# Performance work log

Measured on AMD Instinct MI355X. Metric: run time of the kernel, lower is better.

Reference implementation:

```python
import jax, jax.numpy as jnp
import numpy as np

B, S, D_IN, H, D_OUT = 2048, 256, 3, 128, 6
DT = 0.1


def setup_inputs() -> dict:
    key = jax.random.key(0)
    ks = jax.random.split(key, 7)
    sx = 1.0 / np.sqrt(D_IN)
    sh = 1.0 / np.sqrt(H)
    return {
        "x": jax.random.normal(ks[0], (B, S, D_IN), dtype=jnp.float32),
        "W_xh": jax.random.uniform(ks[1], (H, D_IN), jnp.float32, -sx, sx),
        "W_hh": jax.random.uniform(ks[2], (H, H), jnp.float32, -sh, sh),
        "b_hh": jax.random.uniform(ks[3], (H,), jnp.float32, -sh, sh),
        "log_tau": jnp.zeros((H,), jnp.float32),
        "fc_W": jax.random.uniform(ks[4], (D_OUT, H), jnp.float32, -sh, sh),
        "fc_b": jax.random.uniform(ks[5], (D_OUT,), jnp.float32, -sh, sh),
    }


def reference(x, W_xh, W_hh, b_hh, log_tau, fc_W, fc_b):
    # tau is time-invariant: compute once outside the scan
    tau = jax.nn.softplus(log_tau) + 0.001  # [H]
    # precompute input projections for all timesteps (one big GEMM)
    xp = jnp.einsum("bsd,hd->sbh", x, W_xh)  # [S, B, H]

    def step(h, xt_proj):
        f = jnp.tanh(xt_proj + h @ W_hh.T + b_hh)  # [B, H]
        h = h + (-h + f) / tau * DT
        return h, None

    h0 = jnp.zeros((x.shape[0], W_hh.shape[0]), dtype=x.dtype)
    hT, _ = jax.lax.scan(step, h0, xp)
    params = jax.nn.softplus(hT @ fc_W.T + fc_b)  # [B, 6]
    return params
```

## Files before the change

### kernel.cpp

```cpp
#include <hip/hip_runtime.h>
#include <math.h>

#define B_TOT 2048
#define S_LEN 256
#define DIN   3
#define H     128
#define DOUT  6
#define DT_C  0.1f

#define NROWS 8
#define HPAD  136
#define PPAD  132

#define PRESCALE 2.8853900817779268f

typedef __attribute__((ext_vector_type(8))) short short8;
typedef __attribute__((ext_vector_type(4))) float f32x4;

__device__ __forceinline__ unsigned short f2bf(float f) {
  unsigned int u = __float_as_uint(f);
  u += 0x7FFFu + ((u >> 16) & 1u);
  return (unsigned short)(u >> 16);
}
__device__ __forceinline__ unsigned int pack2_bf16(float a, float b) {
  unsigned int ua = __float_as_uint(a), ub = __float_as_uint(b);
  ua = ua + 0x7FFFu + ((ua >> 16) & 1u);
  ub = ub + 0x7FFFu + ((ub >> 16) & 1u);
  return (ua >> 16) | (ub & 0xFFFF0000u);
}
__device__ __forceinline__ float dpp_xor8(float v) {
  int i = __float_as_int(v);
  int r = __builtin_amdgcn_update_dpp(i, i, 0x128 , 0xF, 0xF, false);
  return __int_as_float(r);
}

__launch_bounds__(512, 2)
__global__ void ltc_kernel(const float* __restrict__ x,
                           const float* __restrict__ W_xh,
                           const float* __restrict__ W_hh,
                           const float* __restrict__ b_hh,
                           const float* __restrict__ log_tau,
                           const float* __restrict__ fc_W,
                           const float* __restrict__ fc_b,
                           float* __restrict__ out) {
  __shared__ alignas(16) unsigned short sh_h[2][NROWS][HPAD];
  __shared__ alignas(16) float sh_p[NROWS][PPAD];

  const int tid  = threadIdx.x;
  const int w    = tid >> 6;
  const int lane = tid & 63;
  const int quad = lane >> 4;
  const int l16  = lane & 15;
  const int rb0  = blockIdx.x * NROWS;

  {
    uint4* p = (uint4*)&sh_h[0][0][0];
    const int n16 = (2 * NROWS * HPAD) / 8;
    for (int i = tid; i < n16; i += 512) p[i] = make_uint4(0, 0, 0, 0);
  }

  short8 wa[4];
  {
    const int j = w * 16 + l16;
#pragma unroll
    for (int kc = 0; kc < 4; ++kc) {
      const float* src = W_hh + j * H + kc * 32 + quad * 8;
#pragma unroll
      for (int i = 0; i < 8; ++i)
        wa[kc][i] = (short)f2bf(src[i] * PRESCALE);
    }
  }

  const int brow = l16 & 7;
  const int rbse = (l16 >> 3) * 2;
  float ewx[2][3], ebh[2], ecc[2], ea[2], encc2[2];
#pragma unroll
  for (int r = 0; r < 2; ++r) {
    const int j = w * 16 + quad * 4 + rbse + r;
    ewx[r][0] = W_xh[j * 3 + 0] * PRESCALE;
    ewx[r][1] = W_xh[j * 3 + 1] * PRESCALE;
    ewx[r][2] = W_xh[j * 3 + 2] * PRESCALE;
    ebh[r]    = b_hh[j] * PRESCALE;
    float lt  = log_tau[j];
    float tau = logf(1.f + expf(lt)) + 0.001f;
    float cc  = DT_C / tau;
    ecc[r]    = cc;
    ea[r]     = 1.f - cc;
    encc2[r]  = -2.f * cc;
  }
  const bool lowhalf = (l16 < 8);
  const float* xp = x + (size_t)(rb0 + brow) * (S_LEN * DIN);

  float hreg[2] = {0.f, 0.f};

  const int rd_off = l16 * HPAD + quad * 8;
  const int wr_off = brow * HPAD + w * 16 + quad * 4 + rbse;
  const unsigned short* __restrict__ buf0 = &sh_h[0][0][0];
  unsigned short* __restrict__ buf1 = &sh_h[1][0][0];

  short8 bf[4];
#pragma unroll
  for (int kc = 0; kc < 4; ++kc) bf[kc] = short8{0, 0, 0, 0, 0, 0, 0, 0};

  float2 pfa = *(const float2*)(xp);
  float2 pfb = *(const float2*)(xp + 2);
  float2 pfc = *(const float2*)(xp + 4);

  __syncthreads();

  auto do_step = [&](const unsigned short* __restrict__ cur,
                     unsigned short* __restrict__ nxt,
                     float xc0, float xc1, float xc2) {
    if (l16 < NROWS) {
#pragma unroll
      for (int kc = 0; kc < 4; ++kc)
        bf[kc] = *(const short8*)(cur + rd_off + kc * 32);
    }

    float t0 = __builtin_fmaf(xc2, ewx[0][2], ebh[0]);
    t0 = __builtin_fmaf(xc1, ewx[0][1], t0);
    t0 = __builtin_fmaf(xc0, ewx[0][0], t0);
    float t1 = __builtin_fmaf(xc2, ewx[1][2], ebh[1]);
    t1 = __builtin_fmaf(xc1, ewx[1][1], t1);
    t1 = __builtin_fmaf(xc0, ewx[1][0], t1);

    f32x4 ah = {0.f, 0.f, 0.f, 0.f};
#pragma unroll
    for (int kc = 0; kc < 4; ++kc)
      ah = __builtin_amdgcn_mfma_f32_16x16x32_bf16(wa[kc], bf[kc], ah, 0, 0, 0);

    float d2 = dpp_xor8(ah[2]);
    float d3 = dpp_xor8(ah[3]);
    float pre0 = lowhalf ? ah[0] : d2;
    float pre1 = lowhalf ? ah[1] : d3;

    {
      float e  = __builtin_amdgcn_exp2f(pre0 + t0);
      float rc = __builtin_amdgcn_rcpf(e + 1.f);
      hreg[0] = __builtin_fmaf(encc2[0], rc, __builtin_fmaf(hreg[0], ea[0], ecc[0]));
    }
    {
      float e  = __builtin_amdgcn_exp2f(pre1 + t1);
      float rc = __builtin_amdgcn_rcpf(e + 1.f);
      hreg[1] = __builtin_fmaf(encc2[1], rc, __builtin_fmaf(hreg[1], ea[1], ecc[1]));
    }

    *(unsigned int*)(nxt + wr_off) = pack2_bf16(hreg[0], hreg[1]);
    __syncthreads();
  };

  for (int s = 0; s < S_LEN; s += 2) {
    float2 xa = pfa, xb = pfb, xc = pfc;
    if (s + 2 < S_LEN) {
      xp += 6;
      pfa = *(const float2*)(xp);
      pfb = *(const float2*)(xp + 2);
      pfc = *(const float2*)(xp + 4);
    }
    do_step(buf0, buf1, xa.x, xa.y, xb.x);
    do_step(buf1, (unsigned short*)buf0, xb.y, xc.x, xc.y);
  }

  {
    float2 v = make_float2(hreg[0], hreg[1]);
    *(float2*)&sh_p[brow][w * 16 + quad * 4 + rbse] = v;
  }
  __syncthreads();

  if (tid < NROWS * DOUT) {
    const int b = tid / DOUT;
    const int o = tid - b * DOUT;
    const float* fw = fc_W + o * H;
    float acc = fc_b[o];
#pragma unroll 4
    for (int k = 0; k < H; ++k) acc += sh_p[b][k] * fw[k];
    float sp = (acc > 15.f) ? acc : logf(1.f + expf(acc));
    out[(rb0 + b) * DOUT + o] = sp;
  }
}

extern "C" void kernel_launch(void* const* d_in, const int* in_sizes, int n_in,
                              void* d_out, int out_size, void* d_ws, size_t ws_size,
                              hipStream_t stream) {
  const float* x       = (const float*)d_in[0];
  const float* W_xh    = (const float*)d_in[1];
  const float* W_hh    = (const float*)d_in[2];
  const float* b_hh    = (const float*)d_in[3];
  const float* log_tau = (const float*)d_in[4];
  const float* fc_W    = (const float*)d_in[5];
  const float* fc_b    = (const float*)d_in[6];
  float* out           = (float*)d_out;

  ltc_kernel<<<dim3(B_TOT / NROWS), dim3(512), 0, stream>>>(
      x, W_xh, W_hh, b_hh, log_tau, fc_W, fc_b, out);
}
```

Before: 144.8 us.

## Halve rows per block, split MFMA chain, one hidden unit per lane

Reduces batch rows per workgroup from 8 to 4, doubling the grid to 512 blocks and raising launch bounds to 4 blocks per CU. Each lane now owns a single hidden unit, extracted from the MFMA accumulators with three DPP rotations and selects. The four dependent MFMAs are split into two independent accumulator chains to shorten latency. Other changes: hardware bf16 conversion, a deeper two-step prefetch of x, and a lighter barrier. It trades more blocks and padding for lower per-step serial latency, and pays with extra DPP/select work and unused MFMA columns.

```diff
diff --git a/kernel.cpp b/kernel.cpp
--- a/kernel.cpp
+++ b/kernel.cpp
@@ -8,8 +8,8 @@
 #define DOUT  6
 #define DT_C  0.1f
 
-#define NROWS 8
-#define HPAD  136
+#define NROWS 4
+#define HPAD  144
 #define PPAD  132
 
 #define PRESCALE 2.8853900817779268f
@@ -17,24 +17,24 @@
 typedef __attribute__((ext_vector_type(8))) short short8;
 typedef __attribute__((ext_vector_type(4))) float f32x4;
 
-__device__ __forceinline__ unsigned short f2bf(float f) {
-  unsigned int u = __float_as_uint(f);
-  u += 0x7FFFu + ((u >> 16) & 1u);
-  return (unsigned short)(u >> 16);
-}
-__device__ __forceinline__ unsigned int pack2_bf16(float a, float b) {
-  unsigned int ua = __float_as_uint(a), ub = __float_as_uint(b);
-  ua = ua + 0x7FFFu + ((ua >> 16) & 1u);
-  ub = ub + 0x7FFFu + ((ub >> 16) & 1u);
-  return (ua >> 16) | (ub & 0xFFFF0000u);
-}
-__device__ __forceinline__ float dpp_xor8(float v) {
+template<int CTRL>
+__device__ __forceinline__ float dpp_rot(float v) {
   int i = __float_as_int(v);
-  int r = __builtin_amdgcn_update_dpp(i, i, 0x128 , 0xF, 0xF, false);
+  int r = __builtin_amdgcn_update_dpp(i, i, CTRL, 0xF, 0xF, false);
   return __int_as_float(r);
 }
 
-__launch_bounds__(512, 2)
+__device__ __forceinline__ unsigned short cvt_bf16(float a) {
+  unsigned int r;
+  asm("v_cvt_pk_bf16_f32 %0, %1, %2" : "=v"(r) : "v"(a), "v"(a));
+  return (unsigned short)r;
+}
+
+__device__ __forceinline__ void lds_barrier() {
+  asm volatile("s_waitcnt lgkmcnt(0)\n\ts_barrier" ::: "memory");
+}
+
+__launch_bounds__(512, 4)
 __global__ void ltc_kernel(const float* __restrict__ x,
                            const float* __restrict__ W_xh,
                            const float* __restrict__ W_hh,
@@ -51,6 +51,8 @@
   const int lane = tid & 63;
   const int quad = lane >> 4;
   const int l16  = lane & 15;
+  const int brow = l16 & 3;
+  const int sel  = l16 >> 2;
   const int rb0  = blockIdx.x * NROWS;
 
   {
@@ -61,110 +63,102 @@
 
   short8 wa[4];
   {
-    const int j = w * 16 + l16;
+    const int jj = w * 16 + l16;
 #pragma unroll
     for (int kc = 0; kc < 4; ++kc) {
-      const float* src = W_hh + j * H + kc * 32 + quad * 8;
+      const float* src = W_hh + jj * H + kc * 32 + quad * 8;
 #pragma unroll
       for (int i = 0; i < 8; ++i)
-        wa[kc][i] = (short)f2bf(src[i] * PRESCALE);
+        wa[kc][i] = (short)cvt_bf16(src[i] * PRESCALE);
     }
   }
 
-  const int brow = l16 & 7;
-  const int rbse = (l16 >> 3) * 2;
-  float ewx[2][3], ebh[2], ecc[2], ea[2], encc2[2];
-#pragma unroll
-  for (int r = 0; r < 2; ++r) {
-    const int j = w * 16 + quad * 4 + rbse + r;
-    ewx[r][0] = W_xh[j * 3 + 0] * PRESCALE;
-    ewx[r][1] = W_xh[j * 3 + 1] * PRESCALE;
-    ewx[r][2] = W_xh[j * 3 + 2] * PRESCALE;
-    ebh[r]    = b_hh[j] * PRESCALE;
-    float lt  = log_tau[j];
-    float tau = logf(1.f + expf(lt)) + 0.001f;
-    float cc  = DT_C / tau;
-    ecc[r]    = cc;
-    ea[r]     = 1.f - cc;
-    encc2[r]  = -2.f * cc;
+  const int j = w * 16 + quad * 4 + sel;
+  const float ewx0 = W_xh[j * 3 + 0] * PRESCALE;
+  const float ewx1 = W_xh[j * 3 + 1] * PRESCALE;
+  const float ewx2 = W_xh[j * 3 + 2] * PRESCALE;
+  const float ebh  = b_hh[j] * PRESCALE;
+  float tau, ecc, ea, encc2;
+  {
+    float lt = log_tau[j];
+    tau   = logf(1.f + expf(lt)) + 0.001f;
+    ecc   = DT_C / tau;
+    ea    = 1.f - ecc;
+    encc2 = -2.f * ecc;
   }
-  const bool lowhalf = (l16 < 8);
-  const float* xp = x + (size_t)(rb0 + brow) * (S_LEN * DIN);
 
-  float hreg[2] = {0.f, 0.f};
+  float hreg = 0.f;
 
-  const int rd_off = l16 * HPAD + quad * 8;
-  const int wr_off = brow * HPAD + w * 16 + quad * 4 + rbse;
-  const unsigned short* __restrict__ buf0 = &sh_h[0][0][0];
+  const int rd_off = brow * HPAD + quad * 8;
+  const int wr_off = brow * HPAD + j;
+  unsigned short* __restrict__ buf0 = &sh_h[0][0][0];
   unsigned short* __restrict__ buf1 = &sh_h[1][0][0];
 
-  short8 bf[4];
-#pragma unroll
-  for (int kc = 0; kc < 4; ++kc) bf[kc] = short8{0, 0, 0, 0, 0, 0, 0, 0};
-
-  float2 pfa = *(const float2*)(xp);
-  float2 pfb = *(const float2*)(xp + 2);
-  float2 pfc = *(const float2*)(xp + 4);
+  const float* xq = x + (size_t)(rb0 + brow) * (S_LEN * DIN);
+  float2 pa0 = *(const float2*)(xq);
+  float2 pb0 = *(const float2*)(xq + 2);
+  float2 pc0 = *(const float2*)(xq + 4);
+  float2 pa1 = *(const float2*)(xq + 6);
+  float2 pb1 = *(const float2*)(xq + 8);
+  float2 pc1 = *(const float2*)(xq + 10);
+  xq += 12;
 
   __syncthreads();
 
-  auto do_step = [&](const unsigned short* __restrict__ cur,
+  auto do_step = [&](unsigned short* __restrict__ cur,
                      unsigned short* __restrict__ nxt,
                      float xc0, float xc1, float xc2) {
-    if (l16 < NROWS) {
-#pragma unroll
-      for (int kc = 0; kc < 4; ++kc)
-        bf[kc] = *(const short8*)(cur + rd_off + kc * 32);
-    }
+    short8 b0 = *(const short8*)(cur + rd_off);
+    short8 b1 = *(const short8*)(cur + rd_off + 32);
+    short8 b2 = *(const short8*)(cur + rd_off + 64);
+    short8 b3 = *(const short8*)(cur + rd_off + 96);
 
-    float t0 = __builtin_fmaf(xc2, ewx[0][2], ebh[0]);
-    t0 = __builtin_fmaf(xc1, ewx[0][1], t0);
-    t0 = __builtin_fmaf(xc0, ewx[0][0], t0);
-    float t1 = __builtin_fmaf(xc2, ewx[1][2], ebh[1]);
-    t1 = __builtin_fmaf(xc1, ewx[1][1], t1);
-    t1 = __builtin_fmaf(xc0, ewx[1][0], t1);
+    float t = __builtin_fmaf(xc2, ewx2, ebh);
+    t = __builtin_fmaf(xc1, ewx1, t);
+    t = __builtin_fmaf(xc0, ewx0, t);
 
-    f32x4 ah = {0.f, 0.f, 0.f, 0.f};
-#pragma unroll
-    for (int kc = 0; kc < 4; ++kc)
-      ah = __builtin_amdgcn_mfma_f32_16x16x32_bf16(wa[kc], bf[kc], ah, 0, 0, 0);
+    f32x4 a0 = {0.f, 0.f, 0.f, 0.f};
+    f32x4 a1 = {0.f, 0.f, 0.f, 0.f};
+    a0 = __builtin_amdgcn_mfma_f32_16x16x32_bf16(wa[0], b0, a0, 0, 0, 0);
+    a1 = __builtin_amdgcn_mfma_f32_16x16x32_bf16(wa[2], b2, a1, 0, 0, 0);
+    a0 = __builtin_amdgcn_mfma_f32_16x16x32_bf16(wa[1], b1, a0, 0, 0, 0);
+    a1 = __builtin_amdgcn_mfma_f32_16x16x32_bf16(wa[3], b3, a1, 0, 0, 0);
 
-    float d2 = dpp_xor8(ah[2]);
-    float d3 = dpp_xor8(ah[3]);
-    float pre0 = lowhalf ? ah[0] : d2;
-    float pre1 = lowhalf ? ah[1] : d3;
+    const float d0 = a0[0] + a1[0];
+    const float d1 = a0[1] + a1[1];
+    const float d2 = a0[2] + a1[2];
+    const float d3 = a0[3] + a1[3];
 
-    {
-      float e  = __builtin_amdgcn_exp2f(pre0 + t0);
-      float rc = __builtin_amdgcn_rcpf(e + 1.f);
-      hreg[0] = __builtin_fmaf(encc2[0], rc, __builtin_fmaf(hreg[0], ea[0], ecc[0]));
-    }
-    {
-      float e  = __builtin_amdgcn_exp2f(pre1 + t1);
-      float rc = __builtin_amdgcn_rcpf(e + 1.f);
-      hreg[1] = __builtin_fmaf(encc2[1], rc, __builtin_fmaf(hreg[1], ea[1], ecc[1]));
-    }
+    float r1 = dpp_rot<0x12C>(d1);
+    float r2 = dpp_rot<0x128>(d2);
+    float r3 = dpp_rot<0x124>(d3);
+    float pre = d0;
+    pre = (sel == 1) ? r1 : pre;
+    pre = (sel == 2) ? r2 : pre;
+    pre = (sel == 3) ? r3 : pre;
 
-    *(unsigned int*)(nxt + wr_off) = pack2_bf16(hreg[0], hreg[1]);
-    __syncthreads();
+    float e  = __builtin_amdgcn_exp2f(pre + t);
+    float rc = __builtin_amdgcn_rcpf(e + 1.f);
+    hreg = __builtin_fmaf(encc2, rc, __builtin_fmaf(hreg, ea, ecc));
+
+    *(unsigned short*)(nxt + wr_off) = cvt_bf16(hreg);
+    lds_barrier();
   };
 
   for (int s = 0; s < S_LEN; s += 2) {
-    float2 xa = pfa, xb = pfb, xc = pfc;
-    if (s + 2 < S_LEN) {
-      xp += 6;
-      pfa = *(const float2*)(xp);
-      pfb = *(const float2*)(xp + 2);
-      pfc = *(const float2*)(xp + 4);
+    float2 xa = pa0, xb = pb0, xc = pc0;
+    pa0 = pa1; pb0 = pb1; pc0 = pc1;
+    if (s + 4 < S_LEN) {
+      pa1 = *(const float2*)(xq);
+      pb1 = *(const float2*)(xq + 2);
+      pc1 = *(const float2*)(xq + 4);
+      xq += 6;
     }
     do_step(buf0, buf1, xa.x, xa.y, xb.x);
-    do_step(buf1, (unsigned short*)buf0, xb.y, xc.x, xc.y);
+    do_step(buf1, buf0, xb.y, xc.x, xc.y);
   }
 
-  {
-    float2 v = make_float2(hreg[0], hreg[1]);
-    *(float2*)&sh_p[brow][w * 16 + quad * 4 + rbse] = v;
-  }
+  sh_p[brow][j] = hreg;
   __syncthreads();
 
   if (tid < NROWS * DOUT) {
```

Measured after the change: 196.4 us. 1.36x slower.

## Swizzle hidden-state LDS layout, split MFMA chains, use hardware bf16 pack and lighter barrier

Applied to the files above, without the earlier changes.

Changes the shared-memory layout of the bf16 hidden state so each MFMA B-operand read is contiguous per quad/lane, removing the padded row layout. Splits the four dependent MFMAs into two independent accumulator chains summed at the end, shortening the per-step dependency latency. Replaces software bf16 rounding with the v_cvt_pk_bf16_f32 instruction and the full __syncthreads with an inline waitcnt+s_barrier. Deepens x prefetch by one more step pair. The inline-asm barrier relies on correct lgkmcnt semantics, and the split adds a few VALU adds per step.

```diff
diff --git a/kernel.cpp b/kernel.cpp
--- a/kernel.cpp
+++ b/kernel.cpp
@@ -9,7 +9,6 @@
 #define DT_C  0.1f
 
 #define NROWS 8
-#define HPAD  136
 #define PPAD  132
 
 #define PRESCALE 2.8853900817779268f
@@ -17,21 +16,20 @@
 typedef __attribute__((ext_vector_type(8))) short short8;
 typedef __attribute__((ext_vector_type(4))) float f32x4;
 
-__device__ __forceinline__ unsigned short f2bf(float f) {
-  unsigned int u = __float_as_uint(f);
-  u += 0x7FFFu + ((u >> 16) & 1u);
-  return (unsigned short)(u >> 16);
-}
-__device__ __forceinline__ unsigned int pack2_bf16(float a, float b) {
-  unsigned int ua = __float_as_uint(a), ub = __float_as_uint(b);
-  ua = ua + 0x7FFFu + ((ua >> 16) & 1u);
-  ub = ub + 0x7FFFu + ((ub >> 16) & 1u);
-  return (ua >> 16) | (ub & 0xFFFF0000u);
-}
 __device__ __forceinline__ float dpp_xor8(float v) {
   int i = __float_as_int(v);
   int r = __builtin_amdgcn_update_dpp(i, i, 0x128 , 0xF, 0xF, false);
   return __int_as_float(r);
+}
+
+__device__ __forceinline__ unsigned int cvt_pk_bf16(float a, float b) {
+  unsigned int r;
+  asm("v_cvt_pk_bf16_f32 %0, %1, %2" : "=v"(r) : "v"(a), "v"(b));
+  return r;
+}
+
+__device__ __forceinline__ void lds_barrier() {
+  asm volatile("s_waitcnt lgkmcnt(0)\n\ts_barrier" ::: "memory");
 }
 
 __launch_bounds__(512, 2)
@@ -43,7 +41,7 @@
                            const float* __restrict__ fc_W,
                            const float* __restrict__ fc_b,
                            float* __restrict__ out) {
-  __shared__ alignas(16) unsigned short sh_h[2][NROWS][HPAD];
+  __shared__ alignas(16) unsigned short sh_h[2][1024];
   __shared__ alignas(16) float sh_p[NROWS][PPAD];
 
   const int tid  = threadIdx.x;
@@ -54,29 +52,32 @@
   const int rb0  = blockIdx.x * NROWS;
 
   {
-    uint4* p = (uint4*)&sh_h[0][0][0];
-    const int n16 = (2 * NROWS * HPAD) / 8;
+    uint4* p = (uint4*)&sh_h[0][0];
+    const int n16 = (2 * 1024) / 8;
     for (int i = tid; i < n16; i += 512) p[i] = make_uint4(0, 0, 0, 0);
   }
 
   short8 wa[4];
   {
-    const int j = w * 16 + l16;
+    const int jj = w * 16 + l16;
 #pragma unroll
     for (int kc = 0; kc < 4; ++kc) {
-      const float* src = W_hh + j * H + kc * 32 + quad * 8;
-#pragma unroll
-      for (int i = 0; i < 8; ++i)
-        wa[kc][i] = (short)f2bf(src[i] * PRESCALE);
+      const float* src = W_hh + jj * H + kc * 32 + quad * 8;
+#pragma unroll
+      for (int i = 0; i < 8; ++i) {
+        unsigned int pk = cvt_pk_bf16(src[i] * PRESCALE, 0.f);
+        wa[kc][i] = (short)(pk & 0xFFFFu);
+      }
     }
   }
 
   const int brow = l16 & 7;
   const int rbse = (l16 >> 3) * 2;
+  const int j0   = w * 16 + quad * 4 + rbse;
   float ewx[2][3], ebh[2], ecc[2], ea[2], encc2[2];
 #pragma unroll
   for (int r = 0; r < 2; ++r) {
-    const int j = w * 16 + quad * 4 + rbse + r;
+    const int j = j0 + r;
     ewx[r][0] = W_xh[j * 3 + 0] * PRESCALE;
     ewx[r][1] = W_xh[j * 3 + 1] * PRESCALE;
     ewx[r][2] = W_xh[j * 3 + 2] * PRESCALE;
@@ -93,18 +94,23 @@
 
   float hreg[2] = {0.f, 0.f};
 
-  const int rd_off = l16 * HPAD + quad * 8;
-  const int wr_off = brow * HPAD + w * 16 + quad * 4 + rbse;
-  const unsigned short* __restrict__ buf0 = &sh_h[0][0][0];
-  unsigned short* __restrict__ buf1 = &sh_h[1][0][0];
+  const int rd_off = quad * 64 + l16 * 8;
+  const int wr_off = (j0 >> 5) * 256 + ((j0 >> 3) & 3) * 64 + brow * 8 + (j0 & 7);
+  unsigned short* __restrict__ buf0 = &sh_h[0][0];
+  unsigned short* __restrict__ buf1 = &sh_h[1][0];
 
   short8 bf[4];
 #pragma unroll
   for (int kc = 0; kc < 4; ++kc) bf[kc] = short8{0, 0, 0, 0, 0, 0, 0, 0};
 
-  float2 pfa = *(const float2*)(xp);
-  float2 pfb = *(const float2*)(xp + 2);
-  float2 pfc = *(const float2*)(xp + 4);
+  const float* xq = xp;
+  float2 pa0 = *(const float2*)(xq);
+  float2 pb0 = *(const float2*)(xq + 2);
+  float2 pc0 = *(const float2*)(xq + 4);
+  float2 pa1 = *(const float2*)(xq + 6);
+  float2 pb1 = *(const float2*)(xq + 8);
+  float2 pc1 = *(const float2*)(xq + 10);
+  xq += 12;
 
   __syncthreads();
 
@@ -114,7 +120,7 @@
     if (l16 < NROWS) {
 #pragma unroll
       for (int kc = 0; kc < 4; ++kc)
-        bf[kc] = *(const short8*)(cur + rd_off + kc * 32);
+        bf[kc] = *(const short8*)(cur + rd_off + kc * 256);
     }
 
     float t0 = __builtin_fmaf(xc2, ewx[0][2], ebh[0]);
@@ -124,15 +130,22 @@
     t1 = __builtin_fmaf(xc1, ewx[1][1], t1);
     t1 = __builtin_fmaf(xc0, ewx[1][0], t1);
 
-    f32x4 ah = {0.f, 0.f, 0.f, 0.f};
-#pragma unroll
-    for (int kc = 0; kc < 4; ++kc)
-      ah = __builtin_amdgcn_mfma_f32_16x16x32_bf16(wa[kc], bf[kc], ah, 0, 0, 0);
-
-    float d2 = dpp_xor8(ah[2]);
-    float d3 = dpp_xor8(ah[3]);
-    float pre0 = lowhalf ? ah[0] : d2;
-    float pre1 = lowhalf ? ah[1] : d3;
+    f32x4 a0 = {0.f, 0.f, 0.f, 0.f};
+    f32x4 a1 = {0.f, 0.f, 0.f, 0.f};
+    a0 = __builtin_amdgcn_mfma_f32_16x16x32_bf16(wa[0], bf[0], a0, 0, 0, 0);
+    a1 = __builtin_amdgcn_mfma_f32_16x16x32_bf16(wa[2], bf[2], a1, 0, 0, 0);
+    a0 = __builtin_amdgcn_mfma_f32_16x16x32_bf16(wa[1], bf[1], a0, 0, 0, 0);
+    a1 = __builtin_amdgcn_mfma_f32_16x16x32_bf16(wa[3], bf[3], a1, 0, 0, 0);
+
+    const float d0 = a0[0] + a1[0];
+    const float d1 = a0[1] + a1[1];
+    const float d2 = a0[2] + a1[2];
+    const float d3 = a0[3] + a1[3];
+
+    float e2 = dpp_xor8(d2);
+    float e3 = dpp_xor8(d3);
+    float pre0 = lowhalf ? d0 : e2;
+    float pre1 = lowhalf ? d1 : e3;
 
     {
       float e  = __builtin_amdgcn_exp2f(pre0 + t0);
@@ -145,25 +158,26 @@
       hreg[1] = __builtin_fmaf(encc2[1], rc, __builtin_fmaf(hreg[1], ea[1], ecc[1]));
     }
 
-    *(unsigned int*)(nxt + wr_off) = pack2_bf16(hreg[0], hreg[1]);
-    __syncthreads();
+    *(unsigned int*)(nxt + wr_off) = cvt_pk_bf16(hreg[0], hreg[1]);
+    lds_barrier();
   };
 
   for (int s = 0; s < S_LEN; s += 2) {
-    float2 xa = pfa, xb = pfb, xc = pfc;
-    if (s + 2 < S_LEN) {
-      xp += 6;
-      pfa = *(const float2*)(xp);
-      pfb = *(const float2*)(xp + 2);
-      pfc = *(const float2*)(xp + 4);
+    float2 xa = pa0, xb = pb0, xc = pc0;
+    pa0 = pa1; pb0 = pb1; pc0 = pc1;
+    if (s + 4 < S_LEN) {
+      pa1 = *(const float2*)(xq);
+      pb1 = *(const float2*)(xq + 2);
+      pc1 = *(const float2*)(xq + 4);
+      xq += 6;
     }
     do_step(buf0, buf1, xa.x, xa.y, xb.x);
-    do_step(buf1, (unsigned short*)buf0, xb.y, xc.x, xc.y);
+    do_step(buf1, buf0, xb.y, xc.x, xc.y);
   }
 
   {
     float2 v = make_float2(hreg[0], hreg[1]);
-    *(float2*)&sh_p[brow][w * 16 + quad * 4 + rbse] = v;
+    *(float2*)&sh_p[brow][j0] = v;
   }
   __syncthreads();
 
```

Result: slower. 186.2 us (+28.6%).

## Process 16 batch rows per block with 4 waves each owning 32 hidden units

Applied to the files above, without the earlier changes.

Each block now handles 16 sequence rows instead of 8 and uses 4 waves instead of 8. Each wave computes two 16-row M-tiles, so the MFMA N dimension is fully used rather than half-padded. The hidden state moves to an unpadded swizzled LDS layout that matches the MFMA B-operand, and the manual bf16 rounding is replaced with the hardware v_cvt_pk_bf16_f32 instruction. The block count halves to 128, so fewer workgroups are spread over the CUs. In exchange there is more per-wave work, with two independent accumulator chains, and fewer barriers per row processed.

```diff
diff --git a/kernel.cpp b/kernel.cpp
--- a/kernel.cpp
+++ b/kernel.cpp
@@ -8,8 +8,7 @@
 #define DOUT  6
 #define DT_C  0.1f
 
-#define NROWS 8
-#define HPAD  136
+#define NROWS 16
 #define PPAD  132
 
 #define PRESCALE 2.8853900817779268f
@@ -17,24 +16,13 @@
 typedef __attribute__((ext_vector_type(8))) short short8;
 typedef __attribute__((ext_vector_type(4))) float f32x4;
 
-__device__ __forceinline__ unsigned short f2bf(float f) {
-  unsigned int u = __float_as_uint(f);
-  u += 0x7FFFu + ((u >> 16) & 1u);
-  return (unsigned short)(u >> 16);
+__device__ __forceinline__ unsigned int cvt_pk_bf16(float a, float b) {
+  unsigned int r;
+  asm("v_cvt_pk_bf16_f32 %0, %1, %2" : "=v"(r) : "v"(a), "v"(b));
+  return r;
 }
-__device__ __forceinline__ unsigned int pack2_bf16(float a, float b) {
-  unsigned int ua = __float_as_uint(a), ub = __float_as_uint(b);
-  ua = ua + 0x7FFFu + ((ua >> 16) & 1u);
-  ub = ub + 0x7FFFu + ((ub >> 16) & 1u);
-  return (ua >> 16) | (ub & 0xFFFF0000u);
-}
-__device__ __forceinline__ float dpp_xor8(float v) {
-  int i = __float_as_int(v);
-  int r = __builtin_amdgcn_update_dpp(i, i, 0x128 , 0xF, 0xF, false);
-  return __int_as_float(r);
-}
-
-__launch_bounds__(512, 2)
+
+__launch_bounds__(256, 1)
 __global__ void ltc_kernel(const float* __restrict__ x,
                            const float* __restrict__ W_xh,
                            const float* __restrict__ W_hh,
@@ -43,7 +31,7 @@
                            const float* __restrict__ fc_W,
                            const float* __restrict__ fc_b,
                            float* __restrict__ out) {
-  __shared__ alignas(16) unsigned short sh_h[2][NROWS][HPAD];
+  __shared__ alignas(16) unsigned short sh_h[2][2048];
   __shared__ alignas(16) float sh_p[NROWS][PPAD];
 
   const int tid  = threadIdx.x;
@@ -54,54 +42,54 @@
   const int rb0  = blockIdx.x * NROWS;
 
   {
-    uint4* p = (uint4*)&sh_h[0][0][0];
-    const int n16 = (2 * NROWS * HPAD) / 8;
-    for (int i = tid; i < n16; i += 512) p[i] = make_uint4(0, 0, 0, 0);
-  }
-
-  short8 wa[4];
-  {
-    const int j = w * 16 + l16;
+    uint4* p = (uint4*)&sh_h[0][0];
+    for (int i = tid; i < 512; i += 256) p[i] = make_uint4(0, 0, 0, 0);
+  }
+
+  short8 wa[2][4];
+#pragma unroll
+  for (int mt = 0; mt < 2; ++mt) {
 #pragma unroll
     for (int kc = 0; kc < 4; ++kc) {
-      const float* src = W_hh + j * H + kc * 32 + quad * 8;
+      const float* src = W_hh + (w * 32 + mt * 16 + l16) * H + kc * 32 + quad * 8;
 #pragma unroll
       for (int i = 0; i < 8; ++i)
-        wa[kc][i] = (short)f2bf(src[i] * PRESCALE);
-    }
-  }
-
-  const int brow = l16 & 7;
-  const int rbse = (l16 >> 3) * 2;
-  float ewx[2][3], ebh[2], ecc[2], ea[2], encc2[2];
-#pragma unroll
-  for (int r = 0; r < 2; ++r) {
-    const int j = w * 16 + quad * 4 + rbse + r;
-    ewx[r][0] = W_xh[j * 3 + 0] * PRESCALE;
-    ewx[r][1] = W_xh[j * 3 + 1] * PRESCALE;
-    ewx[r][2] = W_xh[j * 3 + 2] * PRESCALE;
-    ebh[r]    = b_hh[j] * PRESCALE;
-    float lt  = log_tau[j];
-    float tau = logf(1.f + expf(lt)) + 0.001f;
-    float cc  = DT_C / tau;
-    ecc[r]    = cc;
-    ea[r]     = 1.f - cc;
-    encc2[r]  = -2.f * cc;
-  }
-  const bool lowhalf = (l16 < 8);
-  const float* xp = x + (size_t)(rb0 + brow) * (S_LEN * DIN);
-
-  float hreg[2] = {0.f, 0.f};
-
-  const int rd_off = l16 * HPAD + quad * 8;
-  const int wr_off = brow * HPAD + w * 16 + quad * 4 + rbse;
-  const unsigned short* __restrict__ buf0 = &sh_h[0][0][0];
-  unsigned short* __restrict__ buf1 = &sh_h[1][0][0];
-
-  short8 bf[4];
-#pragma unroll
-  for (int kc = 0; kc < 4; ++kc) bf[kc] = short8{0, 0, 0, 0, 0, 0, 0, 0};
-
+        wa[mt][kc][i] = (short)(cvt_pk_bf16(src[i] * PRESCALE, 0.f) & 0xFFFFu);
+    }
+  }
+
+  float ewx[2][4][3], ebh[2][4], ecc[2][4], ea[2][4], encc2[2][4];
+#pragma unroll
+  for (int mt = 0; mt < 2; ++mt) {
+#pragma unroll
+    for (int r = 0; r < 4; ++r) {
+      const int j = w * 32 + mt * 16 + quad * 4 + r;
+      ewx[mt][r][0] = W_xh[j * 3 + 0] * PRESCALE;
+      ewx[mt][r][1] = W_xh[j * 3 + 1] * PRESCALE;
+      ewx[mt][r][2] = W_xh[j * 3 + 2] * PRESCALE;
+      ebh[mt][r]    = b_hh[j] * PRESCALE;
+      float lt  = log_tau[j];
+      float tau = logf(1.f + expf(lt)) + 0.001f;
+      float cc  = DT_C / tau;
+      ecc[mt][r]   = cc;
+      ea[mt][r]    = 1.f - cc;
+      encc2[mt][r] = -2.f * cc;
+    }
+  }
+
+  float hreg[2][4];
+#pragma unroll
+  for (int mt = 0; mt < 2; ++mt)
+#pragma unroll
+    for (int r = 0; r < 4; ++r) hreg[mt][r] = 0.f;
+
+  const int rd_off  = quad * 128 + l16 * 8;
+  const int wr_off0 = (w * 64 + (0 * 2 + (quad >> 1)) * 16 + l16) * 8 + (quad & 1) * 4;
+  const int wr_off1 = (w * 64 + (1 * 2 + (quad >> 1)) * 16 + l16) * 8 + (quad & 1) * 4;
+  unsigned short* __restrict__ buf0 = &sh_h[0][0];
+  unsigned short* __restrict__ buf1 = &sh_h[1][0];
+
+  const float* xp = x + (size_t)(rb0 + l16) * (S_LEN * DIN);
   float2 pfa = *(const float2*)(xp);
   float2 pfb = *(const float2*)(xp + 2);
   float2 pfc = *(const float2*)(xp + 4);
@@ -111,41 +99,59 @@
   auto do_step = [&](const unsigned short* __restrict__ cur,
                      unsigned short* __restrict__ nxt,
                      float xc0, float xc1, float xc2) {
-    if (l16 < NROWS) {
-#pragma unroll
-      for (int kc = 0; kc < 4; ++kc)
-        bf[kc] = *(const short8*)(cur + rd_off + kc * 32);
-    }
-
-    float t0 = __builtin_fmaf(xc2, ewx[0][2], ebh[0]);
-    t0 = __builtin_fmaf(xc1, ewx[0][1], t0);
-    t0 = __builtin_fmaf(xc0, ewx[0][0], t0);
-    float t1 = __builtin_fmaf(xc2, ewx[1][2], ebh[1]);
-    t1 = __builtin_fmaf(xc1, ewx[1][1], t1);
-    t1 = __builtin_fmaf(xc0, ewx[1][0], t1);
-
-    f32x4 ah = {0.f, 0.f, 0.f, 0.f};
-#pragma unroll
-    for (int kc = 0; kc < 4; ++kc)
-      ah = __builtin_amdgcn_mfma_f32_16x16x32_bf16(wa[kc], bf[kc], ah, 0, 0, 0);
-
-    float d2 = dpp_xor8(ah[2]);
-    float d3 = dpp_xor8(ah[3]);
-    float pre0 = lowhalf ? ah[0] : d2;
-    float pre1 = lowhalf ? ah[1] : d3;
+    short8 b0 = *(const short8*)(cur + rd_off);
+    short8 b1 = *(const short8*)(cur + rd_off + 512);
+    short8 b2 = *(const short8*)(cur + rd_off + 1024);
+    short8 b3 = *(const short8*)(cur + rd_off + 1536);
+
+    float t[2][4];
+#pragma unroll
+    for (int mt = 0; mt < 2; ++mt)
+#pragma unroll
+      for (int r = 0; r < 4; ++r) {
+        float v = __builtin_fmaf(xc2, ewx[mt][r][2], ebh[mt][r]);
+        v = __builtin_fmaf(xc1, ewx[mt][r][1], v);
+        t[mt][r] = __builtin_fmaf(xc0, ewx[mt][r][0], v);
+      }
+
+    f32x4 aA0 = {0.f, 0.f, 0.f, 0.f}, aB0 = {0.f, 0.f, 0.f, 0.f};
+    f32x4 aA1 = {0.f, 0.f, 0.f, 0.f}, aB1 = {0.f, 0.f, 0.f, 0.f};
+    aA0 = __builtin_amdgcn_mfma_f32_16x16x32_bf16(wa[0][0], b0, aA0, 0, 0, 0);
+    aA1 = __builtin_amdgcn_mfma_f32_16x16x32_bf16(wa[1][0], b0, aA1, 0, 0, 0);
+    aB0 = __builtin_amdgcn_mfma_f32_16x16x32_bf16(wa[0][2], b2, aB0, 0, 0, 0);
+    aB1 = __builtin_amdgcn_mfma_f32_16x16x32_bf16(wa[1][2], b2, aB1, 0, 0, 0);
+    aA0 = __builtin_amdgcn_mfma_f32_16x16x32_bf16(wa[0][1], b1, aA0, 0, 0, 0);
+    aA1 = __builtin_amdgcn_mfma_f32_16x16x32_bf16(wa[1][1], b1, aA1, 0, 0, 0);
+    aB0 = __builtin_amdgcn_mfma_f32_16x16x32_bf16(wa[0][3], b3, aB0, 0, 0, 0);
+    aB1 = __builtin_amdgcn_mfma_f32_16x16x32_bf16(wa[1][3], b3, aB1, 0, 0, 0);
+
+#pragma unroll
+    for (int r = 0; r < 4; ++r) {
+      {
+        float pre = aA0[r] + aB0[r];
+        float e   = __builtin_amdgcn_exp2f(pre + t[0][r]);
+        float rc  = __builtin_amdgcn_rcpf(e + 1.f);
+        hreg[0][r] = __builtin_fmaf(encc2[0][r], rc,
+                     __builtin_fmaf(hreg[0][r], ea[0][r], ecc[0][r]));
+      }
+      {
+        float pre = aA1[r] + aB1[r];
+        float e   = __builtin_amdgcn_exp2f(pre + t[1][r]);
+        float rc  = __builtin_amdgcn_rcpf(e + 1.f);
+        hreg[1][r] = __builtin_fmaf(encc2[1][r], rc,
+                     __builtin_fmaf(hreg[1][r], ea[1][r], ecc[1][r]));
+      }
+    }
 
     {
-      float e  = __builtin_amdgcn_exp2f(pre0 + t0);
-      float rc = __builtin_amdgcn_rcpf(e + 1.f);
-      hreg[0] = __builtin_fmaf(encc2[0], rc, __builtin_fmaf(hreg[0], ea[0], ecc[0]));
-    }
-    {
-      float e  = __builtin_amdgcn_exp2f(pre1 + t1);
-      float rc = __builtin_amdgcn_rcpf(e + 1.f);
-      hreg[1] = __builtin_fmaf(encc2[1], rc, __builtin_fmaf(hreg[1], ea[1], ecc[1]));
-    }
-
-    *(unsigned int*)(nxt + wr_off) = pack2_bf16(hreg[0], hreg[1]);
+      uint2 v0, v1;
+      v0.x = cvt_pk_bf16(hreg[0][0], hreg[0][1]);
+      v0.y = cvt_pk_bf16(hreg[0][2], hreg[0][3]);
+      v1.x = cvt_pk_bf16(hreg[1][0], hreg[1][1]);
+      v1.y = cvt_pk_bf16(hreg[1][2], hreg[1][3]);
+      *(uint2*)(nxt + wr_off0) = v0;
+      *(uint2*)(nxt + wr_off1) = v1;
+    }
     __syncthreads();
   };
 
@@ -158,12 +164,14 @@
       pfc = *(const float2*)(xp + 4);
     }
     do_step(buf0, buf1, xa.x, xa.y, xb.x);
-    do_step(buf1, (unsigned short*)buf0, xb.y, xc.x, xc.y);
+    do_step(buf1, buf0, xb.y, xc.x, xc.y);
   }
 
   {
-    float2 v = make_float2(hreg[0], hreg[1]);
-    *(float2*)&sh_p[brow][w * 16 + quad * 4 + rbse] = v;
+    float4 v0 = make_float4(hreg[0][0], hreg[0][1], hreg[0][2], hreg[0][3]);
+    float4 v1 = make_float4(hreg[1][0], hreg[1][1], hreg[1][2], hreg[1][3]);
+    *(float4*)&sh_p[l16][w * 32 + quad * 4]      = v0;
+    *(float4*)&sh_p[l16][w * 32 + 16 + quad * 4] = v1;
   }
   __syncthreads();
 
@@ -191,6 +199,6 @@
   const float* fc_b    = (const float*)d_in[6];
   float* out           = (float*)d_out;
 
-  ltc_kernel<<<dim3(B_TOT / NROWS), dim3(512), 0, stream>>>(
+  ltc_kernel<<<dim3(B_TOT / NROWS), dim3(256), 0, stream>>>(
       x, W_xh, W_hh, b_hh, log_tau, fc_W, fc_b, out);
 }
```

Result: slower. 160.8 us (+11.0%).
